# Kernel tuning notes

Hardware: AMD Instinct MI355X
Metric: run time of the kernel (lower is better)

Reference implementation:

```python
import jax, jax.numpy as jnp
import numpy as np

B, N, D, H = 2, 2048, 1024, 16
HD = D // H
SCALING = HD ** -0.5
# fixed-point quant config (MASE integer quantizer): width=8, frac_width=5 for data/weight/bias
QW, QF = 8, 5


def quantize(x, width=QW, frac_width=QF):
    # MASE integer_quantizer: clamp(round(x * 2^f), -2^(w-1), 2^(w-1)-1) / 2^f
    scale = 2.0 ** frac_width
    xs = x * scale
    rounded = xs + jax.lax.stop_gradient(jnp.round(xs) - xs)  # STE round
    lo = -(2 ** (width - 1))
    hi = 2 ** (width - 1) - 1
    return jnp.clip(rounded, lo, hi) / scale


def linear_integer(x, W, b):
    # quantize activations, weights, bias; then fp matmul of dequantized values
    return quantize(x) @ quantize(W).T + quantize(b)


def bmm_integer(a, b):
    return jnp.einsum('bij,bjk->bik', quantize(a), quantize(b))


def _shape(t):
    # [B, N, D] -> [B*H, N, HD]
    return t.reshape(B, N, H, HD).transpose(0, 2, 1, 3).reshape(B * H, N, HD)


def setup_inputs() -> dict:
    key = jax.random.key(0)
    ks = jax.random.split(key, 9)
    w = lambda k: jax.random.normal(k, (D, D), jnp.float32) * 0.02
    bz = lambda k: jax.random.normal(k, (D,), jnp.float32) * 0.02
    return {
        'hidden_states': jax.random.normal(ks[0], (B, N, D), jnp.float32),
        'attention_mask': jnp.zeros((B, 1, N, N), jnp.float32),
        'q_w': w(ks[1]), 'q_b': bz(ks[2]),
        'k_w': w(ks[3]), 'k_b': bz(ks[4]),
        'v_w': w(ks[5]), 'v_b': bz(ks[6]),
        'o_w': w(ks[7]), 'o_b': bz(ks[8]),
    }


def reference(hidden_states, attention_mask, q_w, q_b, k_w, k_b, v_w, v_b, o_w, o_b):
    q = linear_integer(hidden_states, q_w, q_b) * SCALING          # [B,N,D]
    k = linear_integer(hidden_states, k_w, k_b)
    v = linear_integer(hidden_states, v_w, v_b)
    qh, kh, vh = _shape(q), _shape(k), _shape(v)                   # [B*H,N,HD]

    attn = bmm_integer(qh, kh.transpose(0, 2, 1))                  # [B*H,N,N]
    attn = attn.reshape(B, H, N, N) + attention_mask
    attn = jnp.maximum(attn, jnp.finfo(attn.dtype).min)
    attn = jax.nn.softmax(attn.reshape(B * H, N, N), axis=-1)

    ctx = bmm_integer(attn, vh)                                    # [B*H,N,HD]
    ctx = ctx.reshape(B, H, N, HD).transpose(0, 2, 1, 3).reshape(B, N, D)
    out = linear_integer(ctx, o_w, o_b)
    return out
```

## Files before the change

kernel.cpp:

```cpp
#include <hip/hip_runtime.h>
#include <cstdint>
#include <cfloat>
#include <climits>

#define NB 2
#define NN 2048
#define ND 1024
#define NH 16
#define NHD 64
#define NHB (NB*NH)
#define WS_NEEDED 25186304u

#if defined(__has_builtin)
#if __has_builtin(__builtin_amdgcn_sdot4)
#define HAS_SDOT4 1
#endif
#if __has_builtin(__builtin_amdgcn_exp2f)
#define EXP2F(x) __builtin_amdgcn_exp2f(x)
#else
#define EXP2F(x) exp2f(x)
#endif
#else
#define EXP2F(x) exp2f(x)
#endif

#define C2 0.0014088819735243784f

typedef __attribute__((ext_vector_type(4))) int int32x4;

__device__ __forceinline__ int dot4(int a, int b, int acc) {
#if defined(HAS_SDOT4)
  return __builtin_amdgcn_sdot4(a, b, acc, false);
#else
  acc += (int)(int8_t)(a & 255)       * (int)(int8_t)(b & 255);
  acc += (int)(int8_t)((a >> 8) & 255) * (int)(int8_t)((b >> 8) & 255);
  acc += (int)(int8_t)((a >> 16) & 255)* (int)(int8_t)((b >> 16) & 255);
  acc += (int)(int8_t)(a >> 24)        * (int)(int8_t)(b >> 24);
  return acc;
#endif
}

__device__ __forceinline__ int clampq(int v) {
  return min(127, max(-128, v));
}

__global__ __launch_bounds__(256) void zero_out_k(float4* __restrict__ out) {
  out[blockIdx.x * 256 + threadIdx.x] = float4{0.f, 0.f, 0.f, 0.f};
}

__device__ __forceinline__ int quant4(float4 f) {
  int a = clampq((int)rintf(f.x * 32.f));
  int b = clampq((int)rintf(f.y * 32.f));
  int c = clampq((int)rintf(f.z * 32.f));
  int d = clampq((int)rintf(f.w * 32.f));
  return (a & 255) | ((b & 255) << 8) | ((c & 255) << 16) | (d << 24);
}

__global__ __launch_bounds__(256) void quant_all_k(
    const float* __restrict__ hidden, const float* __restrict__ qw,
    const float* __restrict__ kw, const float* __restrict__ vw,
    const float* __restrict__ ow, const float* __restrict__ qb,
    const float* __restrict__ kb, const float* __restrict__ vb,
    const float* __restrict__ ob, const float* __restrict__ mask,
    int* __restrict__ xo, int* __restrict__ qwo, int* __restrict__ kwo,
    int* __restrict__ vwo, int* __restrict__ owo, int* __restrict__ qbo,
    int* __restrict__ kbo, int* __restrict__ vbo, int* __restrict__ obo,
    int* __restrict__ flags) {
  __shared__ int red[256];
  const int bid = blockIdx.x;
  const int t = threadIdx.x;
  if (bid < 4096) {
    const int i = bid * 256 + t;
    xo[i] = quant4(reinterpret_cast<const float4*>(hidden)[i]);
  } else if (bid < 8192) {
    const int wb = bid - 4096;
    const int which = wb >> 10;
    const float* src = which == 0 ? qw : which == 1 ? kw : which == 2 ? vw : ow;
    int* dst = which == 0 ? qwo : which == 1 ? kwo : which == 2 ? vwo : owo;
    const int i = (wb & 1023) * 256 + t;
    dst[i] = quant4(reinterpret_cast<const float4*>(src)[i]);
  } else if (bid < 8196) {
    const int which = bid - 8192;
    const float* src = which == 0 ? qb : which == 1 ? kb : which == 2 ? vb : ob;
    int* dst = which == 0 ? qbo : which == 1 ? kbo : which == 2 ? vbo : obo;
    dst[t] = quant4(reinterpret_cast<const float4*>(src)[t]);
  } else {
    const int row = bid - 8196;
    const float4* mr = (const float4*)(mask + (size_t)row * NN);
    int nz = 0;
#pragma unroll
    for (int i = 0; i < 2; ++i) {
      float4 f = mr[t * 2 + i];
      nz |= (f.x != 0.f) | (f.y != 0.f) | (f.z != 0.f) | (f.w != 0.f);
    }
    red[t] = nz;
    __syncthreads();
    for (int off = 128; off; off >>= 1) {
      if (t < off) red[t] |= red[t + off];
      __syncthreads();
    }
    if (t == 0) flags[row] = (red[0] == 0);
  }
}

#define BM 64
#define BN 128
#define BK 64

template <bool OPROJ>
__device__ __forceinline__ void gemm_body(const int8_t* __restrict__ x,
                                          const int8_t* __restrict__ w,
                                          const int8_t* __restrict__ bq,
                                          int8_t* __restrict__ outq,
                                          float* __restrict__ outf,
                                          float scale) {
  __shared__ __align__(16) int8_t lA[2][BM * BK];
  __shared__ __align__(16) int8_t lB[2][BN * BK];
  const int t = threadIdx.x;
  const int wid = t >> 6;
  const int lane = t & 63;
  const int wr = wid >> 1, wc = wid & 1;
  const int bm = blockIdx.y * BM;
  const int bn = blockIdx.x * BN;

  const int srow = lane >> 2;
  const int scol = (lane & 3) * 16;
  const int frow = lane & 15;
  const int fk = (lane >> 4) * 16;

  const int8_t* gxa = x + (size_t)(bm + wid * 16 + srow) * ND + scol;
  const int8_t* gwb0 = w + (size_t)(bn + wid * 16 + srow) * ND + scol;
  const int8_t* gwb1 = w + (size_t)(bn + (wid + 4) * 16 + srow) * ND + scol;

#define STAGE(buf, ks)                                                          \
  do {                                                                          \
    const int k0_ = (ks) * BK;                                                  \
    __builtin_amdgcn_global_load_lds(                                           \
        (const __attribute__((address_space(1))) void*)(gxa + k0_),             \
        (__attribute__((address_space(3))) void*)(lA[buf] + wid * 1024), 16, 0, 0); \
    __builtin_amdgcn_global_load_lds(                                           \
        (const __attribute__((address_space(1))) void*)(gwb0 + k0_),            \
        (__attribute__((address_space(3))) void*)(lB[buf] + wid * 1024), 16, 0, 0); \
    __builtin_amdgcn_global_load_lds(                                           \
        (const __attribute__((address_space(1))) void*)(gwb1 + k0_),            \
        (__attribute__((address_space(3))) void*)(lB[buf] + (wid + 4) * 1024), 16, 0, 0); \
  } while (0)

  int32x4 acc[2][4];
#pragma unroll
  for (int i = 0; i < 2; ++i)
#pragma unroll
    for (int j = 0; j < 4; ++j) acc[i][j] = int32x4{0, 0, 0, 0};

  STAGE(0, 0);
  __syncthreads();

  for (int ks = 0; ks < ND / BK; ++ks) {
    const int cur = ks & 1;
    if (ks + 1 < ND / BK) STAGE(cur ^ 1, ks + 1);

    int32x4 af[2], bf[4];
#pragma unroll
    for (int mi = 0; mi < 2; ++mi)
      af[mi] = *(const int32x4*)(lA[cur] + (wr * 32 + mi * 16 + frow) * BK + fk);
#pragma unroll
    for (int ni = 0; ni < 4; ++ni)
      bf[ni] = *(const int32x4*)(lB[cur] + (wc * 64 + ni * 16 + frow) * BK + fk);
#pragma unroll
    for (int mi = 0; mi < 2; ++mi)
#pragma unroll
      for (int ni = 0; ni < 4; ++ni)
        acc[mi][ni] = __builtin_amdgcn_mfma_i32_16x16x64_i8(af[mi], bf[ni],
                                                            acc[mi][ni], 0, 0, 0);
    __syncthreads();
  }
#undef STAGE

  const int crow = (lane >> 4) * 4;
  const int ccol = lane & 15;
#pragma unroll
  for (int ni = 0; ni < 4; ++ni) {
    const int n = bn + wc * 64 + ni * 16 + ccol;
    const float bqf = (float)bq[n] * (1.f / 32.f);
    const int h = n >> 6, hd = n & 63;
#pragma unroll
    for (int mi = 0; mi < 2; ++mi) {
#pragma unroll
      for (int r = 0; r < 4; ++r) {
        const int m = bm + wr * 32 + mi * 16 + crow + r;
        const float val = (float)acc[mi][ni][r] * (1.f / 1024.f) + bqf;
        if (OPROJ) {
          outf[(size_t)m * ND + n] = val;
        } else {
          const int qv = clampq((int)rintf(val * scale * 32.f));
          const int b_ = m >> 11, nr = m & 2047;
          outq[(((size_t)((b_ << 4) + h) << 11) + nr) * NHD + hd] = (int8_t)qv;
        }
      }
    }
  }
}

__global__ __launch_bounds__(256) void gemm_qkv_k(const int8_t* __restrict__ x,
                                                  const int8_t* __restrict__ wq,
                                                  const int8_t* __restrict__ wk,
                                                  const int8_t* __restrict__ wv,
                                                  const int8_t* __restrict__ bqq,
                                                  const int8_t* __restrict__ bqk,
                                                  const int8_t* __restrict__ bqv,
                                                  int8_t* __restrict__ oq,
                                                  int8_t* __restrict__ ok,
                                                  int8_t* __restrict__ ov) {
  const int z = blockIdx.z;
  const int8_t* w = z == 0 ? wq : z == 1 ? wk : wv;
  const int8_t* bq = z == 0 ? bqq : z == 1 ? bqk : bqv;
  int8_t* out = z == 0 ? oq : z == 1 ? ok : ov;
  const float scale = z == 0 ? 0.125f : 1.0f;
  gemm_body<false>(x, w, bq, out, nullptr, scale);
}

__global__ __launch_bounds__(256) void gemm_o_k(const int8_t* __restrict__ x,
                                                const int8_t* __restrict__ w,
                                                const int8_t* __restrict__ bq,
                                                float* __restrict__ out) {
  gemm_body<true>(x, w, bq, nullptr, out, 1.0f);
}

__global__ __launch_bounds__(256) void attn_k(const int8_t* __restrict__ Q,
                                              const int8_t* __restrict__ K,
                                              const int8_t* __restrict__ V,
                                              const float* __restrict__ mask,
                                              const int* __restrict__ flags,
                                              int8_t* __restrict__ ctx) {
  __shared__ float wredf[4][64];
  __shared__ int wredi[4][64];
  __shared__ float sM[64];
  __shared__ int s_dirty[64];
  __shared__ int s_nm;
  __shared__ float sfb[NN];
  __shared__ float fred[256];
  __shared__ int ired[256];
  __shared__ int8_t pq[NN];

  const int t = threadIdx.x;
  const int hb = blockIdx.x, b = hb >> 4, h = hb & 15;
  const int q0 = blockIdx.y * 64;
  const int wid = t >> 6, lane = t & 63;
  const int l15 = lane & 15, l4 = lane >> 4;

  if (t == 0) s_nm = 1;
  __syncthreads();
  if (t < 64 && flags[b * NN + q0 + t] == 0) s_nm = 0;
  __syncthreads();
  const bool nomask = (s_nm != 0);

  const int8_t* Qh = Q + (size_t)hb * NN * NHD;
  const int8_t* Kh = K + (size_t)hb * NN * NHD;

  int32x4 qf0 = *(const int32x4*)(Qh + (size_t)(q0 + l15) * NHD + l4 * 16);
  int32x4 qf1 = *(const int32x4*)(Qh + (size_t)(q0 + 16 + l15) * NHD + l4 * 16);
  int32x4 qf2 = *(const int32x4*)(Qh + (size_t)(q0 + 32 + l15) * NHD + l4 * 16);
  int32x4 qf3 = *(const int32x4*)(Qh + (size_t)(q0 + 48 + l15) * NHD + l4 * 16);

  const float* mr0 = mask + ((size_t)(b * NN + q0 + l15)) * NN;
  const float* mr1 = mr0 + (size_t)16 * NN;
  const float* mr2 = mr0 + (size_t)32 * NN;
  const float* mr3 = mr0 + (size_t)48 * NN;
  const int kwbase = wid * 512;
  const int32x4 z4 = {0, 0, 0, 0};

#define KFRAG(kt) (*(const int32x4*)(Kh + (size_t)(kwbase + (kt) * 16 + l15) * NHD + l4 * 16))

  if (nomask) {
    int im0 = INT_MIN, im1 = INT_MIN, im2 = INT_MIN, im3 = INT_MIN;
    float sa0 = 0.f, sb0 = 0.f, sa1 = 0.f, sb1 = 0.f;
    float sa2 = 0.f, sb2 = 0.f, sa3 = 0.f, sb3 = 0.f;
    int32x4 a = KFRAG(0);
    for (int kt = 0; kt < 32; ++kt) {
      const int32x4 an = KFRAG(kt == 31 ? 31 : kt + 1);
      const int32x4 c0 = __builtin_amdgcn_mfma_i32_16x16x64_i8(a, qf0, z4, 0, 0, 0);
      const int32x4 c1 = __builtin_amdgcn_mfma_i32_16x16x64_i8(a, qf1, z4, 0, 0, 0);
      const int32x4 c2 = __builtin_amdgcn_mfma_i32_16x16x64_i8(a, qf2, z4, 0, 0, 0);
      const int32x4 c3 = __builtin_amdgcn_mfma_i32_16x16x64_i8(a, qf3, z4, 0, 0, 0);
#pragma unroll
      for (int r = 0; r < 4; ++r) {
        im0 = max(im0, c0[r]); im1 = max(im1, c1[r]);
        im2 = max(im2, c2[r]); im3 = max(im3, c3[r]);
      }
      sa0 += EXP2F((float)c0[0] * C2) + EXP2F((float)c0[1] * C2);
      sb0 += EXP2F((float)c0[2] * C2) + EXP2F((float)c0[3] * C2);
      sa1 += EXP2F((float)c1[0] * C2) + EXP2F((float)c1[1] * C2);
      sb1 += EXP2F((float)c1[2] * C2) + EXP2F((float)c1[3] * C2);
      sa2 += EXP2F((float)c2[0] * C2) + EXP2F((float)c2[1] * C2);
      sb2 += EXP2F((float)c2[2] * C2) + EXP2F((float)c2[3] * C2);
      sa3 += EXP2F((float)c3[0] * C2) + EXP2F((float)c3[1] * C2);
      sb3 += EXP2F((float)c3[2] * C2) + EXP2F((float)c3[3] * C2);
      a = an;
    }
    float s0 = sa0 + sb0, s1 = sa1 + sb1, s2 = sa2 + sb2, s3 = sa3 + sb3;
#pragma unroll
    for (int off = 16; off <= 32; off <<= 1) {
      im0 = max(im0, __shfl_xor(im0, off)); s0 += __shfl_xor(s0, off);
      im1 = max(im1, __shfl_xor(im1, off)); s1 += __shfl_xor(s1, off);
      im2 = max(im2, __shfl_xor(im2, off)); s2 += __shfl_xor(s2, off);
      im3 = max(im3, __shfl_xor(im3, off)); s3 += __shfl_xor(s3, off);
    }
    if (lane < 16) {
      wredi[wid][lane] = im0;      wredf[wid][lane] = s0;
      wredi[wid][16 + lane] = im1; wredf[wid][16 + lane] = s1;
      wredi[wid][32 + lane] = im2; wredf[wid][32 + lane] = s2;
      wredi[wid][48 + lane] = im3; wredf[wid][48 + lane] = s3;
    }
    __syncthreads();
    if (t < 64) {
      int M = wredi[0][t];
      float S = wredf[0][t];
#pragma unroll
      for (int w2 = 1; w2 < 4; ++w2) {
        M = max(M, wredi[w2][t]);
        S += wredf[w2][t];
      }
      float lb = (M > 61440 || M < -61440) ? 0.f : S * EXP2F(-(float)M * C2);
      s_dirty[t] = (lb >= 96.f) ? 0 : 1;
    }
    __syncthreads();
  } else {
    float m0 = -FLT_MAX, m1 = -FLT_MAX, m2 = -FLT_MAX, m3 = -FLT_MAX;
    for (int kt = 0; kt < 32; ++kt) {
      const int32x4 a = KFRAG(kt);
      const int32x4 c0 = __builtin_amdgcn_mfma_i32_16x16x64_i8(a, qf0, z4, 0, 0, 0);
      const int32x4 c1 = __builtin_amdgcn_mfma_i32_16x16x64_i8(a, qf1, z4, 0, 0, 0);
      const int32x4 c2 = __builtin_amdgcn_mfma_i32_16x16x64_i8(a, qf2, z4, 0, 0, 0);
      const int32x4 c3 = __builtin_amdgcn_mfma_i32_16x16x64_i8(a, qf3, z4, 0, 0, 0);
      const int kofs = kwbase + kt * 16 + l4 * 4;
#pragma unroll
      for (int r = 0; r < 4; ++r) {
        m0 = fmaxf(m0, fmaxf((float)c0[r] * (1.f / 1024.f) + mr0[kofs + r], -FLT_MAX));
        m1 = fmaxf(m1, fmaxf((float)c1[r] * (1.f / 1024.f) + mr1[kofs + r], -FLT_MAX));
        m2 = fmaxf(m2, fmaxf((float)c2[r] * (1.f / 1024.f) + mr2[kofs + r], -FLT_MAX));
        m3 = fmaxf(m3, fmaxf((float)c3[r] * (1.f / 1024.f) + mr3[kofs + r], -FLT_MAX));
      }
    }
#pragma unroll
    for (int off = 16; off <= 32; off <<= 1) {
      m0 = fmaxf(m0, __shfl_xor(m0, off));
      m1 = fmaxf(m1, __shfl_xor(m1, off));
      m2 = fmaxf(m2, __shfl_xor(m2, off));
      m3 = fmaxf(m3, __shfl_xor(m3, off));
    }
    if (lane < 16) {
      wredf[wid][lane] = m0;      wredf[wid][16 + lane] = m1;
      wredf[wid][32 + lane] = m2; wredf[wid][48 + lane] = m3;
    }
    __syncthreads();
    if (t < 64) {
      float M = wredf[0][t];
#pragma unroll
      for (int w2 = 1; w2 < 4; ++w2) M = fmaxf(M, wredf[w2][t]);
      sM[t] = M;
    }
    __syncthreads();
    const float M0 = sM[l15], M1 = sM[16 + l15];
    const float M2 = sM[32 + l15], M3 = sM[48 + l15];
    float s0 = 0.f, s1 = 0.f, s2 = 0.f, s3 = 0.f;
    for (int kt = 0; kt < 32; ++kt) {
      const int32x4 a = KFRAG(kt);
      const int32x4 c0 = __builtin_amdgcn_mfma_i32_16x16x64_i8(a, qf0, z4, 0, 0, 0);
      const int32x4 c1 = __builtin_amdgcn_mfma_i32_16x16x64_i8(a, qf1, z4, 0, 0, 0);
      const int32x4 c2 = __builtin_amdgcn_mfma_i32_16x16x64_i8(a, qf2, z4, 0, 0, 0);
      const int32x4 c3 = __builtin_amdgcn_mfma_i32_16x16x64_i8(a, qf3, z4, 0, 0, 0);
      const int kofs = kwbase + kt * 16 + l4 * 4;
#pragma unroll
      for (int r = 0; r < 4; ++r) {
        s0 += __expf(fmaxf((float)c0[r] * (1.f / 1024.f) + mr0[kofs + r], -FLT_MAX) - M0);
        s1 += __expf(fmaxf((float)c1[r] * (1.f / 1024.f) + mr1[kofs + r], -FLT_MAX) - M1);
        s2 += __expf(fmaxf((float)c2[r] * (1.f / 1024.f) + mr2[kofs + r], -FLT_MAX) - M2);
        s3 += __expf(fmaxf((float)c3[r] * (1.f / 1024.f) + mr3[kofs + r], -FLT_MAX) - M3);
      }
    }
#pragma unroll
    for (int off = 16; off <= 32; off <<= 1) {
      s0 += __shfl_xor(s0, off); s1 += __shfl_xor(s1, off);
      s2 += __shfl_xor(s2, off); s3 += __shfl_xor(s3, off);
    }
    if (lane < 16) {
      wredf[wid][lane] = s0;      wredf[wid][16 + lane] = s1;
      wredf[wid][32 + lane] = s2; wredf[wid][48 + lane] = s3;
    }
    __syncthreads();
    if (t < 64) {
      const float S = wredf[0][t] + wredf[1][t] + wredf[2][t] + wredf[3][t];
      s_dirty[t] = (S >= 96.f) ? 0 : 1;
    }
    __syncthreads();
  }
#undef KFRAG

  {
    const int rl = t >> 2;
    if (!s_dirty[rl]) {
      int4* p = (int4*)(ctx + ((size_t)(b * NN + q0 + rl)) * ND + h * NHD);
      const int4 z = {0, 0, 0, 0};
      p[(t & 3) * 2] = z;
      p[(t & 3) * 2 + 1] = z;
    }
  }

  for (int rl = 0; rl < 64; ++rl) {
    if (!s_dirty[rl]) continue;
    __syncthreads();
    const int qrow = q0 + rl;
    const int* Qr = (const int*)(Qh + (size_t)qrow * NHD);
    const float* mrow = mask + ((size_t)(b * NN + qrow)) * NN;
    int qreg[16];
#pragma unroll
    for (int i = 0; i < 16; ++i) qreg[i] = Qr[i];
#pragma unroll
    for (int jj = 0; jj < 8; ++jj) {
      const int j = jj * 256 + t;
      const int* Kj = (const int*)(Kh + (size_t)j * NHD);
      int acc = 0;
#pragma unroll
      for (int i = 0; i < 16; ++i) acc = dot4(qreg[i], Kj[i], acc);
      sfb[j] = fmaxf((float)acc * (1.f / 1024.f) + mrow[j], -FLT_MAX);
    }
    __syncthreads();
    float lm = -INFINITY;
#pragma unroll
    for (int jj = 0; jj < 8; ++jj) lm = fmaxf(lm, sfb[jj * 256 + t]);
    fred[t] = lm;
    __syncthreads();
    for (int off = 128; off; off >>= 1) {
      if (t < off) fred[t] = fmaxf(fred[t], fred[t + off]);
      __syncthreads();
    }
    const float M = fred[0];
    __syncthreads();
    float ls = 0.f;
#pragma unroll
    for (int jj = 0; jj < 8; ++jj) {
      const int j = jj * 256 + t;
      const float e = expf(sfb[j] - M);
      sfb[j] = e; ls += e;
    }
    fred[t] = ls;
    __syncthreads();
    for (int off = 128; off; off >>= 1) {
      if (t < off) fred[t] += fred[t + off];
      __syncthreads();
    }
    const float S = fred[0];
#pragma unroll
    for (int jj = 0; jj < 8; ++jj) {
      const int j = jj * 256 + t;
      const int pi = (int)rintf(sfb[j] / S * 32.f);
      pq[j] = (int8_t)min(127, pi);
    }
    __syncthreads();
    const int8_t* Vh = V + (size_t)hb * NN * NHD;
    const int d = t & 63, ch = t >> 6;
    int a = 0;
    for (int j = ch * 512; j < ch * 512 + 512; ++j) {
      const int pv = pq[j];
      if (pv) a += pv * (int)Vh[(size_t)j * NHD + d];
    }
    ired[t] = a;
    __syncthreads();
    if (t < 64) {
      const int tot = ired[t] + ired[t + 64] + ired[t + 128] + ired[t + 192];
      ctx[((size_t)(b * NN + qrow)) * ND + h * NHD + t] =
          (int8_t)clampq((int)rintf((float)tot * (1.f / 32.f)));
    }
    __syncthreads();
  }
}

extern "C" void kernel_launch(void* const* d_in, const int* in_sizes, int n_in,
                              void* d_out, int out_size, void* d_ws, size_t ws_size,
                              hipStream_t stream) {
  float* out = (float*)d_out;

  if (ws_size < (size_t)WS_NEEDED) {
    zero_out_k<<<out_size / 1024, 256, 0, stream>>>((float4*)out);
    return;
  }

  const float* hidden = (const float*)d_in[0];
  const float* mask   = (const float*)d_in[1];
  const float* qw = (const float*)d_in[2];
  const float* qb = (const float*)d_in[3];
  const float* kw = (const float*)d_in[4];
  const float* kb = (const float*)d_in[5];
  const float* vw = (const float*)d_in[6];
  const float* vb = (const float*)d_in[7];
  const float* ow = (const float*)d_in[8];
  const float* ob = (const float*)d_in[9];

  char* ws = (char*)d_ws;
  int8_t* x_i8  = (int8_t*)(ws + 0);
  int8_t* qw_i8 = (int8_t*)(ws + 4194304);
  int8_t* kw_i8 = (int8_t*)(ws + 5242880);
  int8_t* vw_i8 = (int8_t*)(ws + 6291456);
  int8_t* ow_i8 = (int8_t*)(ws + 7340032);
  int8_t* qb_i8 = (int8_t*)(ws + 8388608);
  int8_t* kb_i8 = (int8_t*)(ws + 8389632);
  int8_t* vb_i8 = (int8_t*)(ws + 8390656);
  int8_t* ob_i8 = (int8_t*)(ws + 8391680);
  int8_t* Q_i8  = (int8_t*)(ws + 8392704);
  int8_t* K_i8  = (int8_t*)(ws + 12587008);
  int8_t* V_i8  = (int8_t*)(ws + 16781312);
  int8_t* c_i8  = (int8_t*)(ws + 20975616);
  int* mflags   = (int*)(ws + 25169920);

  quant_all_k<<<12292, 256, 0, stream>>>(hidden, qw, kw, vw, ow, qb, kb, vb, ob,
                                         mask, (int*)x_i8, (int*)qw_i8,
                                         (int*)kw_i8, (int*)vw_i8, (int*)ow_i8,
                                         (int*)qb_i8, (int*)kb_i8, (int*)vb_i8,
                                         (int*)ob_i8, mflags);

  gemm_qkv_k<<<dim3(ND / BN, NB * NN / BM, 3), 256, 0, stream>>>(
      x_i8, qw_i8, kw_i8, vw_i8, qb_i8, kb_i8, vb_i8, Q_i8, K_i8, V_i8);

  attn_k<<<dim3(NHB, NN / 64), 256, 0, stream>>>(Q_i8, K_i8, V_i8, mask, mflags, c_i8);

  gemm_o_k<<<dim3(ND / BN, NB * NN / BM), 256, 0, stream>>>(c_i8, ow_i8, ob_i8, out);
}
```

Measured before the change: 183.8 us.

## Bound softmax via key column sums and skip output projection for clean rows

```diff
diff --git a/kernel.cpp b/kernel.cpp
--- a/kernel.cpp
+++ b/kernel.cpp
@@ -9,22 +9,13 @@
 #define NH 16
 #define NHD 64
 #define NHB (NB*NH)
-#define WS_NEEDED 25186304u
+#define WS_NEEDED 25202688u
 
 #if defined(__has_builtin)
 #if __has_builtin(__builtin_amdgcn_sdot4)
 #define HAS_SDOT4 1
 #endif
-#if __has_builtin(__builtin_amdgcn_exp2f)
-#define EXP2F(x) __builtin_amdgcn_exp2f(x)
-#else
-#define EXP2F(x) exp2f(x)
 #endif
-#else
-#define EXP2F(x) exp2f(x)
-#endif
-
-#define C2 0.0014088819735243784f
 
 typedef __attribute__((ext_vector_type(4))) int int32x4;
 
@@ -65,7 +56,7 @@
     int* __restrict__ xo, int* __restrict__ qwo, int* __restrict__ kwo,
     int* __restrict__ vwo, int* __restrict__ owo, int* __restrict__ qbo,
     int* __restrict__ kbo, int* __restrict__ vbo, int* __restrict__ obo,
-    int* __restrict__ flags) {
+    int* __restrict__ mflags, int* __restrict__ rflags) {
   __shared__ int red[256];
   const int bid = blockIdx.x;
   const int t = threadIdx.x;
@@ -84,7 +75,7 @@
     const float* src = which == 0 ? qb : which == 1 ? kb : which == 2 ? vb : ob;
     int* dst = which == 0 ? qbo : which == 1 ? kbo : which == 2 ? vbo : obo;
     dst[t] = quant4(reinterpret_cast<const float4*>(src)[t]);
-  } else {
+  } else if (bid < 12292) {
     const int row = bid - 8196;
     const float4* mr = (const float4*)(mask + (size_t)row * NN);
     int nz = 0;
@@ -99,7 +90,10 @@
       if (t < off) red[t] |= red[t + off];
       __syncthreads();
     }
-    if (t == 0) flags[row] = (red[0] == 0);
+    if (t == 0) mflags[row] = (red[0] == 0);
+  } else {
+#pragma unroll
+    for (int i = 0; i < 16; ++i) rflags[t * 16 + i] = 0;
   }
 }
 
@@ -222,7 +216,31 @@
 __global__ __launch_bounds__(256) void gemm_o_k(const int8_t* __restrict__ x,
                                                 const int8_t* __restrict__ w,
                                                 const int8_t* __restrict__ bq,
+                                                const int* __restrict__ rflags,
                                                 float* __restrict__ out) {
+  __shared__ int s_any;
+  const int t = threadIdx.x;
+  const int bm = blockIdx.y * BM;
+  const int bn = blockIdx.x * BN;
+  if (t == 0) s_any = 0;
+  __syncthreads();
+  if (t < 64 && rflags[bm + t] != 0) s_any = 1;
+  __syncthreads();
+  if (s_any == 0) {
+    const int m = bm + (t >> 2);
+    const int n0 = bn + (t & 3) * 32;
+    float4* po = (float4*)(out + (size_t)m * ND + n0);
+#pragma unroll
+    for (int j = 0; j < 8; ++j) {
+      float4 v;
+      v.x = (float)bq[n0 + j * 4 + 0] * (1.f / 32.f);
+      v.y = (float)bq[n0 + j * 4 + 1] * (1.f / 32.f);
+      v.z = (float)bq[n0 + j * 4 + 2] * (1.f / 32.f);
+      v.w = (float)bq[n0 + j * 4 + 3] * (1.f / 32.f);
+      po[j] = v;
+    }
+    return;
+  }
   gemm_body<true>(x, w, bq, nullptr, out, 1.0f);
 }
 
@@ -230,17 +248,14 @@
                                               const int8_t* __restrict__ K,
                                               const int8_t* __restrict__ V,
                                               const float* __restrict__ mask,
-                                              const int* __restrict__ flags,
-                                              int8_t* __restrict__ ctx) {
-  __shared__ float wredf[4][64];
+                                              const int* __restrict__ mflags,
+                                              int8_t* __restrict__ ctx,
+                                              int* __restrict__ rflags) {
+  __shared__ __align__(16) char pool[16384];
+  __shared__ int sKsum[64];
+  __shared__ long long sQdK[64];
   __shared__ int wredi[4][64];
-  __shared__ float sM[64];
   __shared__ int s_dirty[64];
-  __shared__ int s_nm;
-  __shared__ float sfb[NN];
-  __shared__ float fred[256];
-  __shared__ int ired[256];
-  __shared__ int8_t pq[NN];
 
   const int t = threadIdx.x;
   const int hb = blockIdx.x, b = hb >> 4, h = hb & 15;
@@ -248,33 +263,58 @@
   const int wid = t >> 6, lane = t & 63;
   const int l15 = lane & 15, l4 = lane >> 4;
 
-  if (t == 0) s_nm = 1;
-  __syncthreads();
-  if (t < 64 && flags[b * NN + q0 + t] == 0) s_nm = 0;
-  __syncthreads();
-  const bool nomask = (s_nm != 0);
-
   const int8_t* Qh = Q + (size_t)hb * NN * NHD;
   const int8_t* Kh = K + (size_t)hb * NN * NHD;
-
-  int32x4 qf0 = *(const int32x4*)(Qh + (size_t)(q0 + l15) * NHD + l4 * 16);
-  int32x4 qf1 = *(const int32x4*)(Qh + (size_t)(q0 + 16 + l15) * NHD + l4 * 16);
-  int32x4 qf2 = *(const int32x4*)(Qh + (size_t)(q0 + 32 + l15) * NHD + l4 * 16);
-  int32x4 qf3 = *(const int32x4*)(Qh + (size_t)(q0 + 48 + l15) * NHD + l4 * 16);
-
-  const float* mr0 = mask + ((size_t)(b * NN + q0 + l15)) * NN;
-  const float* mr1 = mr0 + (size_t)16 * NN;
-  const float* mr2 = mr0 + (size_t)32 * NN;
-  const float* mr3 = mr0 + (size_t)48 * NN;
+  const int8_t* Vh = V + (size_t)hb * NN * NHD;
+
+  {
+    int (*part)[64] = (int(*)[64])pool;
+    const int rgrp = t >> 2, sl = t & 3;
+    int a[16];
+#pragma unroll
+    for (int j = 0; j < 16; ++j) a[j] = 0;
+    for (int i = 0; i < 32; ++i) {
+      const int row = rgrp + (i << 6);
+      const int4 v = *(const int4*)(Kh + (size_t)row * NHD + sl * 16);
+      const int vv[4] = {v.x, v.y, v.z, v.w};
+#pragma unroll
+      for (int c = 0; c < 4; ++c) {
+        a[c * 4 + 0] += (int)(int8_t)(vv[c] & 255);
+        a[c * 4 + 1] += (int)(int8_t)((vv[c] >> 8) & 255);
+        a[c * 4 + 2] += (int)(int8_t)((vv[c] >> 16) & 255);
+        a[c * 4 + 3] += (int)(int8_t)(vv[c] >> 24);
+      }
+    }
+#pragma unroll
+    for (int j = 0; j < 16; ++j) part[rgrp][sl * 16 + j] = a[j];
+    __syncthreads();
+    if (t < 64) {
+      int s = 0;
+#pragma unroll 8
+      for (int rg = 0; rg < 64; ++rg) s += part[rg][t];
+      sKsum[t] = s;
+    }
+    __syncthreads();
+  }
+
+  if (t < 64) {
+    const int8_t* qr = Qh + (size_t)(q0 + t) * NHD;
+    long long s = 0;
+#pragma unroll 16
+    for (int d = 0; d < 64; ++d) s += (long long)qr[d] * (long long)sKsum[d];
+    sQdK[t] = s;
+  }
+
+  const int32x4 qf0 = *(const int32x4*)(Qh + (size_t)(q0 + l15) * NHD + l4 * 16);
+  const int32x4 qf1 = *(const int32x4*)(Qh + (size_t)(q0 + 16 + l15) * NHD + l4 * 16);
+  const int32x4 qf2 = *(const int32x4*)(Qh + (size_t)(q0 + 32 + l15) * NHD + l4 * 16);
+  const int32x4 qf3 = *(const int32x4*)(Qh + (size_t)(q0 + 48 + l15) * NHD + l4 * 16);
   const int kwbase = wid * 512;
   const int32x4 z4 = {0, 0, 0, 0};
-
 #define KFRAG(kt) (*(const int32x4*)(Kh + (size_t)(kwbase + (kt) * 16 + l15) * NHD + l4 * 16))
 
-  if (nomask) {
-    int im0 = INT_MIN, im1 = INT_MIN, im2 = INT_MIN, im3 = INT_MIN;
-    float sa0 = 0.f, sb0 = 0.f, sa1 = 0.f, sb1 = 0.f;
-    float sa2 = 0.f, sb2 = 0.f, sa3 = 0.f, sb3 = 0.f;
+  int im0 = INT_MIN, im1 = INT_MIN, im2 = INT_MIN, im3 = INT_MIN;
+  {
     int32x4 a = KFRAG(0);
     for (int kt = 0; kt < 32; ++kt) {
       const int32x4 an = KFRAG(kt == 31 ? 31 : kt + 1);
@@ -282,130 +322,52 @@
       const int32x4 c1 = __builtin_amdgcn_mfma_i32_16x16x64_i8(a, qf1, z4, 0, 0, 0);
       const int32x4 c2 = __builtin_amdgcn_mfma_i32_16x16x64_i8(a, qf2, z4, 0, 0, 0);
       const int32x4 c3 = __builtin_amdgcn_mfma_i32_16x16x64_i8(a, qf3, z4, 0, 0, 0);
-#pragma unroll
-      for (int r = 0; r < 4; ++r) {
-        im0 = max(im0, c0[r]); im1 = max(im1, c1[r]);
-        im2 = max(im2, c2[r]); im3 = max(im3, c3[r]);
-      }
-      sa0 += EXP2F((float)c0[0] * C2) + EXP2F((float)c0[1] * C2);
-      sb0 += EXP2F((float)c0[2] * C2) + EXP2F((float)c0[3] * C2);
-      sa1 += EXP2F((float)c1[0] * C2) + EXP2F((float)c1[1] * C2);
-      sb1 += EXP2F((float)c1[2] * C2) + EXP2F((float)c1[3] * C2);
-      sa2 += EXP2F((float)c2[0] * C2) + EXP2F((float)c2[1] * C2);
-      sb2 += EXP2F((float)c2[2] * C2) + EXP2F((float)c2[3] * C2);
-      sa3 += EXP2F((float)c3[0] * C2) + EXP2F((float)c3[1] * C2);
-      sb3 += EXP2F((float)c3[2] * C2) + EXP2F((float)c3[3] * C2);
+      im0 = max(im0, max(max(c0[0], c0[1]), max(c0[2], c0[3])));
+      im1 = max(im1, max(max(c1[0], c1[1]), max(c1[2], c1[3])));
+      im2 = max(im2, max(max(c2[0], c2[1]), max(c2[2], c2[3])));
+      im3 = max(im3, max(max(c3[0], c3[1]), max(c3[2], c3[3])));
       a = an;
     }
-    float s0 = sa0 + sb0, s1 = sa1 + sb1, s2 = sa2 + sb2, s3 = sa3 + sb3;
-#pragma unroll
-    for (int off = 16; off <= 32; off <<= 1) {
-      im0 = max(im0, __shfl_xor(im0, off)); s0 += __shfl_xor(s0, off);
-      im1 = max(im1, __shfl_xor(im1, off)); s1 += __shfl_xor(s1, off);
-      im2 = max(im2, __shfl_xor(im2, off)); s2 += __shfl_xor(s2, off);
-      im3 = max(im3, __shfl_xor(im3, off)); s3 += __shfl_xor(s3, off);
-    }
-    if (lane < 16) {
-      wredi[wid][lane] = im0;      wredf[wid][lane] = s0;
-      wredi[wid][16 + lane] = im1; wredf[wid][16 + lane] = s1;
-      wredi[wid][32 + lane] = im2; wredf[wid][32 + lane] = s2;
-      wredi[wid][48 + lane] = im3; wredf[wid][48 + lane] = s3;
-    }
-    __syncthreads();
-    if (t < 64) {
-      int M = wredi[0][t];
-      float S = wredf[0][t];
-#pragma unroll
-      for (int w2 = 1; w2 < 4; ++w2) {
-        M = max(M, wredi[w2][t]);
-        S += wredf[w2][t];
-      }
-      float lb = (M > 61440 || M < -61440) ? 0.f : S * EXP2F(-(float)M * C2);
-      s_dirty[t] = (lb >= 96.f) ? 0 : 1;
-    }
-    __syncthreads();
-  } else {
-    float m0 = -FLT_MAX, m1 = -FLT_MAX, m2 = -FLT_MAX, m3 = -FLT_MAX;
-    for (int kt = 0; kt < 32; ++kt) {
-      const int32x4 a = KFRAG(kt);
-      const int32x4 c0 = __builtin_amdgcn_mfma_i32_16x16x64_i8(a, qf0, z4, 0, 0, 0);
-      const int32x4 c1 = __builtin_amdgcn_mfma_i32_16x16x64_i8(a, qf1, z4, 0, 0, 0);
-      const int32x4 c2 = __builtin_amdgcn_mfma_i32_16x16x64_i8(a, qf2, z4, 0, 0, 0);
-      const int32x4 c3 = __builtin_amdgcn_mfma_i32_16x16x64_i8(a, qf3, z4, 0, 0, 0);
-      const int kofs = kwbase + kt * 16 + l4 * 4;
-#pragma unroll
-      for (int r = 0; r < 4; ++r) {
-        m0 = fmaxf(m0, fmaxf((float)c0[r] * (1.f / 1024.f) + mr0[kofs + r], -FLT_MAX));
-        m1 = fmaxf(m1, fmaxf((float)c1[r] * (1.f / 1024.f) + mr1[kofs + r], -FLT_MAX));
-        m2 = fmaxf(m2, fmaxf((float)c2[r] * (1.f / 1024.f) + mr2[kofs + r], -FLT_MAX));
-        m3 = fmaxf(m3, fmaxf((float)c3[r] * (1.f / 1024.f) + mr3[kofs + r], -FLT_MAX));
-      }
-    }
-#pragma unroll
-    for (int off = 16; off <= 32; off <<= 1) {
-      m0 = fmaxf(m0, __shfl_xor(m0, off));
-      m1 = fmaxf(m1, __shfl_xor(m1, off));
-      m2 = fmaxf(m2, __shfl_xor(m2, off));
-      m3 = fmaxf(m3, __shfl_xor(m3, off));
-    }
-    if (lane < 16) {
-      wredf[wid][lane] = m0;      wredf[wid][16 + lane] = m1;
-      wredf[wid][32 + lane] = m2; wredf[wid][48 + lane] = m3;
-    }
-    __syncthreads();
-    if (t < 64) {
-      float M = wredf[0][t];
-#pragma unroll
-      for (int w2 = 1; w2 < 4; ++w2) M = fmaxf(M, wredf[w2][t]);
-      sM[t] = M;
-    }
-    __syncthreads();
-    const float M0 = sM[l15], M1 = sM[16 + l15];
-    const float M2 = sM[32 + l15], M3 = sM[48 + l15];
-    float s0 = 0.f, s1 = 0.f, s2 = 0.f, s3 = 0.f;
-    for (int kt = 0; kt < 32; ++kt) {
-      const int32x4 a = KFRAG(kt);
-      const int32x4 c0 = __builtin_amdgcn_mfma_i32_16x16x64_i8(a, qf0, z4, 0, 0, 0);
-      const int32x4 c1 = __builtin_amdgcn_mfma_i32_16x16x64_i8(a, qf1, z4, 0, 0, 0);
-      const int32x4 c2 = __builtin_amdgcn_mfma_i32_16x16x64_i8(a, qf2, z4, 0, 0, 0);
-      const int32x4 c3 = __builtin_amdgcn_mfma_i32_16x16x64_i8(a, qf3, z4, 0, 0, 0);
-      const int kofs = kwbase + kt * 16 + l4 * 4;
-#pragma unroll
-      for (int r = 0; r < 4; ++r) {
-        s0 += __expf(fmaxf((float)c0[r] * (1.f / 1024.f) + mr0[kofs + r], -FLT_MAX) - M0);
-        s1 += __expf(fmaxf((float)c1[r] * (1.f / 1024.f) + mr1[kofs + r], -FLT_MAX) - M1);
-        s2 += __expf(fmaxf((float)c2[r] * (1.f / 1024.f) + mr2[kofs + r], -FLT_MAX) - M2);
-        s3 += __expf(fmaxf((float)c3[r] * (1.f / 1024.f) + mr3[kofs + r], -FLT_MAX) - M3);
-      }
-    }
-#pragma unroll
-    for (int off = 16; off <= 32; off <<= 1) {
-      s0 += __shfl_xor(s0, off); s1 += __shfl_xor(s1, off);
-      s2 += __shfl_xor(s2, off); s3 += __shfl_xor(s3, off);
-    }
-    if (lane < 16) {
-      wredf[wid][lane] = s0;      wredf[wid][16 + lane] = s1;
-      wredf[wid][32 + lane] = s2; wredf[wid][48 + lane] = s3;
-    }
-    __syncthreads();
-    if (t < 64) {
-      const float S = wredf[0][t] + wredf[1][t] + wredf[2][t] + wredf[3][t];
-      s_dirty[t] = (S >= 96.f) ? 0 : 1;
-    }
-    __syncthreads();
   }
 #undef KFRAG
+#pragma unroll
+  for (int off = 16; off <= 32; off <<= 1) {
+    im0 = max(im0, __shfl_xor(im0, off));
+    im1 = max(im1, __shfl_xor(im1, off));
+    im2 = max(im2, __shfl_xor(im2, off));
+    im3 = max(im3, __shfl_xor(im3, off));
+  }
+  if (lane < 16) {
+    wredi[wid][lane] = im0;      wredi[wid][16 + lane] = im1;
+    wredi[wid][32 + lane] = im2; wredi[wid][48 + lane] = im3;
+  }
+  __syncthreads();
+
+  if (t < 64) {
+    int M = wredi[0][t];
+#pragma unroll
+    for (int w2 = 1; w2 < 4; ++w2) M = max(M, wredi[w2][t]);
+    const int gr = b * NN + q0 + t;
+    const bool ok = (mflags[gr] != 0) &&
+                    ((long long)M * 2048LL - sQdK[t] <= 6963200LL);
+    s_dirty[t] = ok ? 0 : 1;
+    if (!ok) atomicOr(&rflags[gr], 1);
+  }
+  __syncthreads();
 
   {
     const int rl = t >> 2;
     if (!s_dirty[rl]) {
       int4* p = (int4*)(ctx + ((size_t)(b * NN + q0 + rl)) * ND + h * NHD);
       const int4 z = {0, 0, 0, 0};
-      p[(t & 3) * 2] = z;
-      p[(t & 3) * 2 + 1] = z;
-    }
-  }
-
+      p[t & 3] = z;
+    }
+  }
+
+  float* sfb = (float*)pool;
+  int8_t* pq = (int8_t*)(pool + 8192);
+  float* fred = (float*)(pool + 10240);
+  int* ired = (int*)(pool + 11264);
   for (int rl = 0; rl < 64; ++rl) {
     if (!s_dirty[rl]) continue;
     __syncthreads();
@@ -457,7 +419,6 @@
       pq[j] = (int8_t)min(127, pi);
     }
     __syncthreads();
-    const int8_t* Vh = V + (size_t)hb * NN * NHD;
     const int d = t & 63, ch = t >> 6;
     int a = 0;
     for (int j = ch * 512; j < ch * 512 + 512; ++j) {
@@ -511,17 +472,20 @@
   int8_t* V_i8  = (int8_t*)(ws + 16781312);
   int8_t* c_i8  = (int8_t*)(ws + 20975616);
   int* mflags   = (int*)(ws + 25169920);
-
-  quant_all_k<<<12292, 256, 0, stream>>>(hidden, qw, kw, vw, ow, qb, kb, vb, ob,
+  int* rflags   = (int*)(ws + 25186304);
+
+  quant_all_k<<<12293, 256, 0, stream>>>(hidden, qw, kw, vw, ow, qb, kb, vb, ob,
                                          mask, (int*)x_i8, (int*)qw_i8,
                                          (int*)kw_i8, (int*)vw_i8, (int*)ow_i8,
                                          (int*)qb_i8, (int*)kb_i8, (int*)vb_i8,
-                                         (int*)ob_i8, mflags);
+                                         (int*)ob_i8, mflags, rflags);
 
   gemm_qkv_k<<<dim3(ND / BN, NB * NN / BM, 3), 256, 0, stream>>>(
       x_i8, qw_i8, kw_i8, vw_i8, qb_i8, kb_i8, vb_i8, Q_i8, K_i8, V_i8);
 
-  attn_k<<<dim3(NHB, NN / 64), 256, 0, stream>>>(Q_i8, K_i8, V_i8, mask, mflags, c_i8);
-
-  gemm_o_k<<<dim3(ND / BN, NB * NN / BM), 256, 0, stream>>>(c_i8, ow_i8, ob_i8, out);
-}
+  attn_k<<<dim3(NHB, NN / 64), 256, 0, stream>>>(Q_i8, K_i8, V_i8, mask, mflags,
+                                                 c_i8, rflags);
+
+  gemm_o_k<<<dim3(ND / BN, NB * NN / BM), 256, 0, stream>>>(c_i8, ow_i8, ob_i8,
+                                                            rflags, out);
+}
```

Result: faster. 171.3 us (-6.8%).
